# Performance work log

Hardware: AMD Instinct MI355X
Metric: run time of the kernel (lower is better)

## Reference

```python
import jax, jax.numpy as jnp
import numpy as np

B = 65536
HID = 256
C_K, C_V, C_S, NQ = 4, 8, 4, 4
EMB_OUT = 64  # state_embedding_size - 1


def _spatial_basis():
    # h = w = 5, U = V = 2 -> [5,5,4] Fourier basis
    ph = jnp.arange(1.0, 6.0)[:, None] * jnp.ones((1, 5)) * (np.pi / 5.0)
    pw = jnp.ones((5, 1)) * jnp.arange(1.0, 6.0)[None, :] * (np.pi / 5.0)
    u = jnp.arange(1.0, 3.0)[None, :]
    a = jnp.cos(ph[:, :, None] * u)  # [5,5,2]
    b = jnp.cos(pw[:, :, None] * u)  # [5,5,2]
    return jnp.einsum('hwu,hwv->hwuv', a, b).reshape(5, 5, 4).astype(jnp.float32)


def _conv(x, w, b):
    # x: NHWC, w: HWIO, pad=1, stride=1
    y = jax.lax.conv_general_dilated(x, w, window_strides=(1, 1), padding=[(1, 1), (1, 1)],
                                     dimension_numbers=('NHWC', 'HWIO', 'NHWC'))
    return y + b


def setup_inputs() -> dict:
    key = jax.random.key(0)
    ks = jax.random.split(key, 20)
    s = 0.05
    inp = {
        'X': jax.random.normal(ks[0], (B, 7, 7, 3), jnp.float32),
        'upper_module_hidden_state': jax.random.normal(ks[1], (B, HID), jnp.float32),
        'c1_w': jax.random.normal(ks[2], (5, 5, 3, 8), jnp.float32) * s,
        'c1_b': jax.random.normal(ks[3], (8,), jnp.float32) * s,
        'c2_w': jax.random.normal(ks[4], (3, 3, 8, 12), jnp.float32) * s,
        'c2_b': jax.random.normal(ks[5], (12,), jnp.float32) * s,
    }
    qdims = [(HID, 256), (256, 128), (128, 64), (64, 32), (32, 32)]
    for i, (din, dout) in enumerate(qdims):
        inp[f'qw{i}'] = jax.random.normal(ks[6 + 2 * i], (din, dout), jnp.float32) * s
        inp[f'qb{i}'] = jax.random.normal(ks[7 + 2 * i], (dout,), jnp.float32) * s
    inp['aw0'] = jax.random.normal(ks[16], ((C_V + C_S) * NQ, 32), jnp.float32) * s
    inp['ab0'] = jax.random.normal(ks[17], (32,), jnp.float32) * s
    inp['aw1'] = jax.random.normal(ks[18], (32, EMB_OUT), jnp.float32) * s
    inp['ab1'] = jax.random.normal(ks[19], (EMB_OUT,), jnp.float32) * s
    return inp


def reference(X, upper_module_hidden_state, c1_w, c1_b, c2_w, c2_b,
              qw0, qb0, qw1, qb1, qw2, qb2, qw3, qb3, qw4, qb4,
              aw0, ab0, aw1, ab1):
    b = X.shape[0]
    # vision CNN: [b,7,7,3] -> [b,5,5,8] -> [b,5,5,12]
    O = _conv(_conv(X, c1_w, c1_b), c2_w, c2_b)
    K, V = O[..., :C_K], O[..., C_K:]
    S = jnp.broadcast_to(_spatial_basis(), (b, 5, 5, C_S))
    K = jnp.concatenate([K, S], axis=-1)  # [b,5,5,8]
    V = jnp.concatenate([V, S], axis=-1)  # [b,5,5,12]
    # query MLP -> [b,4,8]
    q = upper_module_hidden_state
    for w, bi in [(qw0, qb0), (qw1, qb1), (qw2, qb2), (qw3, qb3)]:
        q = jax.nn.relu(q @ w + bi)
    q = (q @ qw4 + qb4).reshape(-1, NQ, C_K + C_S)
    # attention logits over 25 spatial positions, softmax over space
    A = jnp.einsum('bhwk,bqk->bhwq', K, q).reshape(b, 25, NQ)
    A = jax.nn.softmax(A, axis=1)
    # apply_alpha: [b,nq,25] @ [b,25,12] -> [b,nq,12]; chunk+cat == reshape
    a = jnp.einsum('bpq,bpd->bqd', A, V.reshape(b, 25, C_V + C_S)).reshape(b, NQ * (C_V + C_S))
    # answer MLP
    return jax.nn.relu(a @ aw0 + ab0) @ aw1 + ab1
```

## Files before the change

kernel.cpp:

```cpp
#include <hip/hip_runtime.h>
#include <hip/hip_bf16.h>

#define NB 65536

typedef __attribute__((ext_vector_type(8))) short short8;
typedef __attribute__((ext_vector_type(4))) short short4v;
typedef __attribute__((ext_vector_type(4))) float f32x4;
typedef __attribute__((ext_vector_type(16))) float f32x16;
typedef __attribute__((ext_vector_type(4))) unsigned int u32x4;

__device__ inline short f2bf(float f) {
    unsigned u = __builtin_bit_cast(unsigned, f);
    unsigned r = (u + 0x7fffu + ((u >> 16) & 1u)) >> 16;
    return (short)(unsigned short)r;
}
__device__ inline float b2f(short s) {
    return __builtin_bit_cast(float, (unsigned)((unsigned short)s) << 16);
}
__device__ inline unsigned pkbf(float lo, float hi) {
    return ((unsigned)(unsigned short)f2bf(hi) << 16) | (unsigned)(unsigned short)f2bf(lo);
}

#define MLPW_CNT 109568
#define WEFF_CNT 51200
#define A0 (MLPW_CNT + WEFF_CNT + 320)
#define A1 (A0 + 2048)
#define A2 (A1 + 2048)
#define A3 (A2 + 100)
#define PREP_TOT (A3 + 512)


__global__ void __launch_bounds__(256) prep_kernel(
    const float* __restrict__ w0, const float* __restrict__ w1,
    const float* __restrict__ w2, const float* __restrict__ w3,
    const float* __restrict__ w4,
    const float* __restrict__ b0, const float* __restrict__ b1,
    const float* __restrict__ b2, const float* __restrict__ b3,
    const float* __restrict__ b4,
    const float* __restrict__ c1w, const float* __restrict__ c1b,
    const float* __restrict__ c2w, const float* __restrict__ c2b,
    const float* __restrict__ aw0, const float* __restrict__ aw1,
    short* __restrict__ wt, short* __restrict__ weff, float* __restrict__ beff,
    short* __restrict__ aw0T, short* __restrict__ aw1T, float* __restrict__ sTab,
    float* __restrict__ biasP)
{
    int idx = blockIdx.x * 256 + threadIdx.x;
    if (idx < MLPW_CNT) {
        const float* W; int N, KT, base;
        if (idx < 65536)       { W = w0; N = 256; KT = 16; base = 0; }
        else if (idx < 98304)  { W = w1; N = 128; KT = 16; base = 65536; }
        else if (idx < 106496) { W = w2; N = 64;  KT = 8;  base = 98304; }
        else if (idx < 108544) { W = w3; N = 32;  KT = 4;  base = 106496; }
        else                   { W = w4; N = 32;  KT = 2;  base = 108544; }
        int i  = idx - base;
        int nt = i / (KT * 512);
        int r1 = i - nt * (KT * 512);
        int kt = r1 >> 9;
        int l  = (r1 & 511) >> 3;
        int j  = i & 7;
        int n  = nt * 32 + (l & 31);
        int k  = kt * 16 + ((l >> 5) << 3) + j;
        wt[idx] = f2bf(W[k * N + n]);
    } else if (idx < MLPW_CNT + WEFF_CNT) {
        int it = idx - MLPW_CNT;
        int n = it / 160, k = it - n * 160;
        float acc = 0.f;
        if (n < 300 && k < 147) {
            int oc = n % 12, p = n / 12, oy = p / 5, ox = p - oy * 5;
            int ci = k % 3,  t = k / 3, iy = t / 7, ix = t - iy * 7;
            for (int y = 0; y < 5; ++y) {
                int ky = iy - y + 1, ly = y - oy + 1;
                if ((unsigned)ky < 5u && (unsigned)ly < 3u) {
                    for (int x = 0; x < 5; ++x) {
                        int kx = ix - x + 1, lx = x - ox + 1;
                        if ((unsigned)kx < 5u && (unsigned)lx < 3u) {
                            const float* p1 = c1w + ((ky * 5 + kx) * 3 + ci) * 8;
                            const float* p2 = c2w + ((ly * 3 + lx) * 8) * 12 + oc;
#pragma unroll
                            for (int c = 0; c < 8; ++c) acc += p1[c] * p2[c * 12];
                        }
                    }
                }
            }
        }
        weff[it] = f2bf(acc);
    } else if (idx < A0) {
        int n = idx - MLPW_CNT - WEFF_CNT;
        float acc = 0.f;
        if (n < 300) {
            int oc = n % 12, p = n / 12, oy = p / 5, ox = p - oy * 5;
            acc = c2b[oc];
            for (int y = 0; y < 5; ++y) {
                int ly = y - oy + 1;
                if ((unsigned)ly < 3u) {
                    for (int x = 0; x < 5; ++x) {
                        int lx = x - ox + 1;
                        if ((unsigned)lx < 3u) {
#pragma unroll
                            for (int c = 0; c < 8; ++c)
                                acc += c2w[((ly * 3 + lx) * 8 + c) * 12 + oc] * c1b[c];
                        }
                    }
                }
            }
        }
        beff[n] = acc;
    } else if (idx < A1) {
        int t = idx - A0;
        int n = t >> 6, k = t & 63;
        aw0T[t] = (k < 48) ? f2bf(aw0[k * 32 + n]) : (short)0;
    } else if (idx < A2) {
        int t = idx - A1;
        int n = t >> 5, k = t & 31;
        aw1T[t] = f2bf(aw1[k * 64 + n]);
    } else if (idx < A3) {
        int i = idx - A2;
        int p = i >> 2, s = i & 3;
        int h = p / 5, w = p - 5 * h;
        int u = (s >> 1) + 1, v = (s & 1) + 1;
        const float PI5 = 0.6283185307179586f;
        sTab[i] = cosf(((float)(h + 1) * PI5) * (float)u) *
                  cosf(((float)(w + 1) * PI5) * (float)v);
    } else if (idx < PREP_TOT) {
        int t = idx - A3;
        const float* B; int N, base;
        if (t < 256)      { B = b0; N = 256; base = 0; }
        else if (t < 384) { B = b1; N = 128; base = 256; }
        else if (t < 448) { B = b2; N = 64;  base = 384; }
        else if (t < 480) { B = b3; N = 32;  base = 448; }
        else              { B = b4; N = 32;  base = 480; }
        int u  = t - base;
        int h  = u / (N / 2);
        int w  = u - h * (N / 2);
        int nt = w >> 4, r = w & 15;
        biasP[t] = B[nt * 32 + (r & 3) + 8 * (r >> 2) + 4 * h];
    }
}

template<int K, int N, bool RELU>
__device__ inline void layerR(const short* __restrict__ wp,
                              const float* __restrict__ bp,
                              const u32x4* __restrict__ inF,
                              u32x4* __restrict__ outF,
                              int lane, int h)
{
    constexpr int KT = K / 16, NT = N / 32;
#pragma unroll
    for (int nt = 0; nt < NT; ++nt) {
        f32x16 a;
#pragma unroll
        for (int r = 0; r < 16; ++r) a[r] = 0.f;
#pragma unroll
        for (int kt = 0; kt < KT; ++kt) {
            short8 wf = *(const short8*)(wp + (nt * KT + kt) * 512 + lane * 8);
            a = __builtin_amdgcn_mfma_f32_32x32x16_bf16(
                    wf, __builtin_bit_cast(short8, inF[kt]), a, 0, 0, 0);
        }
        const float* bpp = bp + h * (N / 2) + nt * 16;
        unsigned q[8];
#pragma unroll
        for (int i = 0; i < 8; ++i) {
            float v0 = a[2 * i] + bpp[2 * i];
            float v1 = a[2 * i + 1] + bpp[2 * i + 1];
            if (RELU) { v0 = fmaxf(v0, 0.f); v1 = fmaxf(v1, 0.f); }
            q[i] = pkbf(v0, v1);
        }
        unsigned xq[8];
#pragma unroll
        for (int i = 0; i < 8; ++i) xq[i] = (unsigned)__shfl_xor((int)q[i], 32, 64);
        u32x4 fa, fb;
        if (h == 0) {
            fa[0] = q[0];  fa[1] = q[1];  fa[2] = xq[0]; fa[3] = xq[1];
            fb[0] = q[4];  fb[1] = q[5];  fb[2] = xq[4]; fb[3] = xq[5];
        } else {
            fa[0] = xq[2]; fa[1] = xq[3]; fa[2] = q[2];  fa[3] = q[3];
            fb[0] = xq[6]; fb[1] = xq[7]; fb[2] = q[6];  fb[3] = q[7];
        }
        outF[2 * nt]     = fa;
        outF[2 * nt + 1] = fb;
    }
}

template<int K>
__device__ inline void layerQ(const short* __restrict__ wp,
                              const float* __restrict__ bp,
                              const u32x4* __restrict__ inF,
                              short* __restrict__ qout,
                              int lane, int h, int r0)
{
    constexpr int KT = K / 16;
    f32x16 a;
#pragma unroll
    for (int r = 0; r < 16; ++r) a[r] = 0.f;
#pragma unroll
    for (int kt = 0; kt < KT; ++kt) {
        short8 wf = *(const short8*)(wp + kt * 512 + lane * 8);
        a = __builtin_amdgcn_mfma_f32_32x32x16_bf16(
                wf, __builtin_bit_cast(short8, inF[kt]), a, 0, 0, 0);
    }
    const float* bpp = bp + h * 16;
    short* qb = qout + (size_t)(r0 + (lane & 31)) * 32 + 4 * h;
    const int fo[8] = {0, 2, 8, 10, 16, 18, 24, 26};
#pragma unroll
    for (int i = 0; i < 8; ++i) {
        float v0 = a[2 * i] + bpp[2 * i];
        float v1 = a[2 * i + 1] + bpp[2 * i + 1];
        *(unsigned*)(qb + fo[i]) = pkbf(v0, v1);
    }
}

__global__ void __launch_bounds__(64, 2) mlp_kernel(
    const float* __restrict__ hid,
    const short* __restrict__ wp,
    const float* __restrict__ biasP,
    short* __restrict__ qout)
{
    const int lane = threadIdx.x;
    const int h = lane >> 5, b = lane & 31;
    const int r0 = blockIdx.x * 32;

    u32x4 A[16], B[16], C[8], D[4], E[2];
    const float* hb = hid + (size_t)(r0 + b) * 256 + h * 8;
#pragma unroll
    for (int kt = 0; kt < 16; ++kt) {
        float4 x = *(const float4*)(hb + kt * 16);
        float4 y = *(const float4*)(hb + kt * 16 + 4);
        u32x4 f;
        f[0] = pkbf(x.x, x.y); f[1] = pkbf(x.z, x.w);
        f[2] = pkbf(y.x, y.y); f[3] = pkbf(y.z, y.w);
        A[kt] = f;
    }
    layerR<256, 256, true>(wp,          biasP,       A, B, lane, h);
    layerR<256, 128, true>(wp + 65536,  biasP + 256, B, C, lane, h);
    layerR<128,  64, true>(wp + 98304,  biasP + 384, C, D, lane, h);
    layerR< 64,  32, true>(wp + 106496, biasP + 448, D, E, lane, h);
    layerQ< 32>           (wp + 108544, biasP + 480, E, qout, lane, h, r0);
}

__global__ void __launch_bounds__(64) conv_attn_kernel(
    const float* __restrict__ Xg,
    const short* __restrict__ weffT,
    const float* __restrict__ beff,
    const short* __restrict__ aw0T, const float* __restrict__ ab0,
    const short* __restrict__ aw1T, const float* __restrict__ ab1,
    const float* __restrict__ sTab,
    const short* __restrict__ qb16,
    float* __restrict__ out)
{
    __shared__ __align__(16) unsigned char spool[14096];
    short* sKc = (short*)spool;
    short* sVc = (short*)(spool + 3200);
    short* sX  = (short*)spool;
    short* sQ  = (short*)(spool + 9600);
    float* sS  = (float*)(spool + 10624);
    short* sA  = (short*)(spool + 11024);
    short* sH  = (short*)(spool + 13072);

    const int lane   = threadIdx.x;
    const int lanelo = lane & 15;
    const int g      = lane >> 4;
    const int blk    = blockIdx.x;

    {
        short8 qv = *(const short8*)(qb16 + blk * 512 + lane * 8);
        *(short8*)(sQ + lane * 8) = qv;
    }
    if (lane < 50) {
        float2 t = *(const float2*)(sTab + lane * 2);
        sS[lane * 2]     = t.x;
        sS[lane * 2 + 1] = t.y;
    }
#pragma unroll
    for (int i = 0; i < 4; ++i) {
        int t = lane + i * 64;
        if (t < 208) {
            int r = t / 13, c = 147 + (t - r * 13);
            int ch = c >> 3;
            sX[r * 192 + ((ch ^ (r & 7)) << 3) + (c & 7)] = 0;
        }
    }
    {
        const float* xb = Xg + (size_t)blk * 2352;
#define PUTX(IDX, F) { int _i = (IDX); int _r = _i / 147; int _c = _i - _r * 147; \
        int _ch = _c >> 3; sX[_r * 192 + ((_ch ^ (_r & 7)) << 3) + (_c & 7)] = f2bf(F); }
#pragma unroll
        for (int i = 0; i < 10; ++i) {
            int idx4 = lane + i * 64;
            if (idx4 < 588) {
                float4 v = reinterpret_cast<const float4*>(xb)[idx4];
                int base = idx4 * 4;
                PUTX(base + 0, v.x)
                PUTX(base + 1, v.y)
                PUTX(base + 2, v.z)
                PUTX(base + 3, v.w)
            }
        }
#undef PUTX
    }

    short8 af[5];
#pragma unroll
    for (int kt = 0; kt < 5; ++kt) {
        int phys = (kt * 4 + g) ^ (lanelo & 7);
        af[kt] = *(const short8*)(sX + lanelo * 192 + phys * 8);
    }

    short8 bf[2][5];
    {
        const short* wb = weffT + lanelo * 160 + g * 8;
#pragma unroll
        for (int kt = 0; kt < 5; ++kt) bf[0][kt] = *(const short8*)(wb + kt * 32);
    }
#pragma unroll
    for (int nt = 0; nt < 19; ++nt) {
        if (nt + 1 < 19) {
            const short* wb = weffT + ((nt + 1) * 16 + lanelo) * 160 + g * 8;
#pragma unroll
            for (int kt = 0; kt < 5; ++kt)
                bf[(nt + 1) & 1][kt] = *(const short8*)(wb + kt * 32);
        }
        f32x4 a; a[0] = 0.f; a[1] = 0.f; a[2] = 0.f; a[3] = 0.f;
#pragma unroll
        for (int kt = 0; kt < 5; ++kt)
            a = __builtin_amdgcn_mfma_f32_16x16x32_bf16(af[kt], bf[nt & 1][kt], a, 0, 0, 0);
        int n = nt * 16 + lanelo;
        if (n < 300) {
            float bb = beff[n];
            int p = n / 12, c = n - p * 12;
#pragma unroll
            for (int j = 0; j < 4; ++j) {
                int el = g * 4 + j;
                float v = a[j] + bb;
                if (c < 4) sKc[el * 100 + p * 4 + c]       = f2bf(v);
                else       sVc[el * 200 + p * 8 + (c - 4)] = f2bf(v);
            }
        }
    }

    {
        const int el = lane >> 2, qi = lane & 3;
        short8 qv = *(const short8*)(sQ + el * 32 + qi * 8);
        float qf[8];
#pragma unroll
        for (int i = 0; i < 8; ++i) qf[i] = b2f(qv[i]);

        float lg[25];
        float mx = -1e30f;
#pragma unroll
        for (int p = 0; p < 25; ++p) {
            short4v kv = *(const short4v*)(sKc + el * 100 + p * 4);
            const float* sp = sS + p * 4;
            float s = b2f(kv[0]) * qf[0] + b2f(kv[1]) * qf[1]
                    + b2f(kv[2]) * qf[2] + b2f(kv[3]) * qf[3]
                    + sp[0] * qf[4] + sp[1] * qf[5]
                    + sp[2] * qf[6] + sp[3] * qf[7];
            lg[p] = s;
            mx = fmaxf(mx, s);
        }
        float sum = 0.f;
#pragma unroll
        for (int p = 0; p < 25; ++p) { lg[p] = __expf(lg[p] - mx); sum += lg[p]; }
        float inv = 1.f / sum;

        float o[12];
#pragma unroll
        for (int d = 0; d < 12; ++d) o[d] = 0.f;
#pragma unroll
        for (int p = 0; p < 25; ++p) {
            float w = lg[p];
            short4v v0 = *(const short4v*)(sVc + el * 200 + p * 8);
            short4v v1 = *(const short4v*)(sVc + el * 200 + p * 8 + 4);
            const float* sp = sS + p * 4;
            o[0] += w * b2f(v0[0]); o[1] += w * b2f(v0[1]);
            o[2] += w * b2f(v0[2]); o[3] += w * b2f(v0[3]);
            o[4] += w * b2f(v1[0]); o[5] += w * b2f(v1[1]);
            o[6] += w * b2f(v1[2]); o[7] += w * b2f(v1[3]);
            o[8]  += w * sp[0]; o[9]  += w * sp[1];
            o[10] += w * sp[2]; o[11] += w * sp[3];
        }
#pragma unroll
        for (int d = 0; d < 12; ++d) {
            int col = qi * 12 + d;
            int ch = col >> 3;
            sA[el * 64 + ((ch ^ (el & 7)) << 3) + (col & 7)] = f2bf(o[d] * inv);
        }
#pragma unroll
        for (int t = 0; t < 4; ++t) {
            int col = 48 + qi * 4 + t;
            int ch = col >> 3;
            sA[el * 64 + ((ch ^ (el & 7)) << 3) + (col & 7)] = 0;
        }
    }

    {
        short8 aa0, aa1;
        {
            int p0 = (0 * 4 + g) ^ (lanelo & 7);
            int p1 = (1 * 4 + g) ^ (lanelo & 7);
            aa0 = *(const short8*)(sA + lanelo * 64 + p0 * 8);
            aa1 = *(const short8*)(sA + lanelo * 64 + p1 * 8);
        }
#pragma unroll
        for (int nt2 = 0; nt2 < 2; ++nt2) {
            int n = nt2 * 16 + lanelo;
            short8 bw0 = *(const short8*)(aw0T + n * 64 + g * 8);
            short8 bw1 = *(const short8*)(aw0T + n * 64 + 32 + g * 8);
            f32x4 hh; hh[0] = 0.f; hh[1] = 0.f; hh[2] = 0.f; hh[3] = 0.f;
            hh = __builtin_amdgcn_mfma_f32_16x16x32_bf16(aa0, bw0, hh, 0, 0, 0);
            hh = __builtin_amdgcn_mfma_f32_16x16x32_bf16(aa1, bw1, hh, 0, 0, 0);
            float bb = ab0[n];
#pragma unroll
            for (int j = 0; j < 4; ++j) {
                int row = g * 4 + j;
                int ch = n >> 3;
                float v = fmaxf(hh[j] + bb, 0.f);
                sH[row * 32 + ((ch ^ (row & 3)) << 3) + (n & 7)] = f2bf(v);
            }
        }
    }

    {
        short8 ah;
        {
            int ph = (g ^ (lanelo & 3));
            ah = *(const short8*)(sH + lanelo * 32 + ph * 8);
        }
#pragma unroll
        for (int nt3 = 0; nt3 < 4; ++nt3) {
            int n = nt3 * 16 + lanelo;
            short8 bw = *(const short8*)(aw1T + n * 32 + g * 8);
            f32x4 oacc; oacc[0] = 0.f; oacc[1] = 0.f; oacc[2] = 0.f; oacc[3] = 0.f;
            oacc = __builtin_amdgcn_mfma_f32_16x16x32_bf16(ah, bw, oacc, 0, 0, 0);
            float bb = ab1[n];
#pragma unroll
            for (int j = 0; j < 4; ++j) {
                int el = g * 4 + j;
                out[((size_t)blk * 16 + el) * 64 + n] = oacc[j] + bb;
            }
        }
    }
}


extern "C" void kernel_launch(void* const* d_in, const int* in_sizes, int n_in,
                              void* d_out, int out_size, void* d_ws, size_t ws_size,
                              hipStream_t stream)
{
    const float* X   = (const float*)d_in[0];
    const float* hid = (const float*)d_in[1];
    const float* c1w = (const float*)d_in[2];
    const float* c1b = (const float*)d_in[3];
    const float* c2w = (const float*)d_in[4];
    const float* c2b = (const float*)d_in[5];
    const float* qw0 = (const float*)d_in[6];
    const float* qb0 = (const float*)d_in[7];
    const float* qw1 = (const float*)d_in[8];
    const float* qb1 = (const float*)d_in[9];
    const float* qw2 = (const float*)d_in[10];
    const float* qb2 = (const float*)d_in[11];
    const float* qw3 = (const float*)d_in[12];
    const float* qb3 = (const float*)d_in[13];
    const float* qw4 = (const float*)d_in[14];
    const float* qb4 = (const float*)d_in[15];
    const float* aw0 = (const float*)d_in[16];
    const float* ab0 = (const float*)d_in[17];
    const float* aw1 = (const float*)d_in[18];
    const float* ab1 = (const float*)d_in[19];

    float* out   = (float*)d_out;
    short* qb16  = (short*)d_ws;
    short* wsW   = qb16 + (size_t)NB * 32;
    short* weffT = wsW + MLPW_CNT;
    float* beff  = (float*)(weffT + WEFF_CNT);
    short* aw0T  = (short*)(beff + 320);
    short* aw1T  = aw0T + 2048;
    float* sTab  = (float*)(aw1T + 2048);
    float* biasP = sTab + 100;

    hipLaunchKernelGGL(prep_kernel, dim3((PREP_TOT + 255) / 256), dim3(256), 0, stream,
                       qw0, qw1, qw2, qw3, qw4, qb0, qb1, qb2, qb3, qb4,
                       c1w, c1b, c2w, c2b, aw0, aw1,
                       wsW, weffT, beff, aw0T, aw1T, sTab, biasP);
    hipLaunchKernelGGL(mlp_kernel, dim3(NB / 32), dim3(64), 0, stream,
                       hid, wsW, biasP, qb16);
    hipLaunchKernelGGL(conv_attn_kernel, dim3(NB / 16), dim3(64), 0, stream,
                       X, weffT, beff, aw0T, ab0, aw1T, ab1, sTab, qb16, out);
}
```

Baseline: 89.47 us.

## Process two 16-element tiles per conv_attn block to reuse conv weights

The conv/attention kernel now handles 32 batch elements per 64-thread block instead of 16. Each loaded conv weight fragment feeds two MFMAs, one per tile, and weight prefetch is deepened to triple buffering. The grid is halved, and the query and spatial-table staging through shared memory is replaced with direct global loads. In exchange, register pressure and shared memory per block roughly double, with a launch-bounds hint of two blocks, which may reduce occupancy.

```diff
diff --git a/kernel.cpp b/kernel.cpp
--- a/kernel.cpp
+++ b/kernel.cpp
@@ -237,7 +237,7 @@
     layerQ< 32>           (wp + 108544, biasP + 480, E, qout, lane, h, r0);
 }
 
-__global__ void __launch_bounds__(64) conv_attn_kernel(
+__global__ void __launch_bounds__(64, 2) conv_attn_kernel(
     const float* __restrict__ Xg,
     const short* __restrict__ weffT,
     const float* __restrict__ beff,
@@ -247,40 +247,28 @@
     const short* __restrict__ qb16,
     float* __restrict__ out)
 {
-    __shared__ __align__(16) unsigned char spool[14096];
-    short* sKc = (short*)spool;
-    short* sVc = (short*)(spool + 3200);
-    short* sX  = (short*)spool;
-    short* sQ  = (short*)(spool + 9600);
-    float* sS  = (float*)(spool + 10624);
-    short* sA  = (short*)(spool + 11024);
-    short* sH  = (short*)(spool + 13072);
+    __shared__ __align__(16) short sKV[2][4800];
+    __shared__ __align__(16) short sA[2][1024];
+    __shared__ __align__(16) short sH[2][512];
 
     const int lane   = threadIdx.x;
     const int lanelo = lane & 15;
     const int g      = lane >> 4;
     const int blk    = blockIdx.x;
 
-    {
-        short8 qv = *(const short8*)(qb16 + blk * 512 + lane * 8);
-        *(short8*)(sQ + lane * 8) = qv;
-    }
-    if (lane < 50) {
-        float2 t = *(const float2*)(sTab + lane * 2);
-        sS[lane * 2]     = t.x;
-        sS[lane * 2 + 1] = t.y;
-    }
-#pragma unroll
-    for (int i = 0; i < 4; ++i) {
-        int t = lane + i * 64;
-        if (t < 208) {
-            int r = t / 13, c = 147 + (t - r * 13);
-            int ch = c >> 3;
-            sX[r * 192 + ((ch ^ (r & 7)) << 3) + (c & 7)] = 0;
-        }
-    }
-    {
-        const float* xb = Xg + (size_t)blk * 2352;
+#pragma unroll
+    for (int t = 0; t < 2; ++t) {
+        short* sX = &sKV[t][0];
+#pragma unroll
+        for (int i = 0; i < 4; ++i) {
+            int tt = lane + i * 64;
+            if (tt < 208) {
+                int r = tt / 13, c = 147 + (tt - r * 13);
+                int ch = c >> 3;
+                sX[r * 192 + ((ch ^ (r & 7)) << 3) + (c & 7)] = 0;
+            }
+        }
+        const float* xb = Xg + (size_t)blk * 4704 + t * 2352;
 #define PUTX(IDX, F) { int _i = (IDX); int _r = _i / 147; int _c = _i - _r * 147; \
         int _ch = _c >> 3; sX[_r * 192 + ((_ch ^ (_r & 7)) << 3) + (_c & 7)] = f2bf(F); }
 #pragma unroll
@@ -298,48 +286,68 @@
 #undef PUTX
     }
 
-    short8 af[5];
+    short8 af0[5], af1[5];
 #pragma unroll
     for (int kt = 0; kt < 5; ++kt) {
         int phys = (kt * 4 + g) ^ (lanelo & 7);
-        af[kt] = *(const short8*)(sX + lanelo * 192 + phys * 8);
-    }
-
-    short8 bf[2][5];
+        af0[kt] = *(const short8*)(&sKV[0][0] + lanelo * 192 + phys * 8);
+        af1[kt] = *(const short8*)(&sKV[1][0] + lanelo * 192 + phys * 8);
+    }
+
+    short8 bf[3][5];
     {
-        const short* wb = weffT + lanelo * 160 + g * 8;
-#pragma unroll
-        for (int kt = 0; kt < 5; ++kt) bf[0][kt] = *(const short8*)(wb + kt * 32);
+        const short* wb0 = weffT + lanelo * 160 + g * 8;
+        const short* wb1 = weffT + (16 + lanelo) * 160 + g * 8;
+#pragma unroll
+        for (int kt = 0; kt < 5; ++kt) {
+            bf[0][kt] = *(const short8*)(wb0 + kt * 32);
+            bf[1][kt] = *(const short8*)(wb1 + kt * 32);
+        }
     }
 #pragma unroll
     for (int nt = 0; nt < 19; ++nt) {
-        if (nt + 1 < 19) {
-            const short* wb = weffT + ((nt + 1) * 16 + lanelo) * 160 + g * 8;
+        if (nt + 2 < 19) {
+            const short* wb = weffT + ((nt + 2) * 16 + lanelo) * 160 + g * 8;
 #pragma unroll
             for (int kt = 0; kt < 5; ++kt)
-                bf[(nt + 1) & 1][kt] = *(const short8*)(wb + kt * 32);
-        }
-        f32x4 a; a[0] = 0.f; a[1] = 0.f; a[2] = 0.f; a[3] = 0.f;
-#pragma unroll
-        for (int kt = 0; kt < 5; ++kt)
-            a = __builtin_amdgcn_mfma_f32_16x16x32_bf16(af[kt], bf[nt & 1][kt], a, 0, 0, 0);
+                bf[(nt + 2) % 3][kt] = *(const short8*)(wb + kt * 32);
+        }
+        f32x4 a0, a1;
+        a0[0] = 0.f; a0[1] = 0.f; a0[2] = 0.f; a0[3] = 0.f;
+        a1[0] = 0.f; a1[1] = 0.f; a1[2] = 0.f; a1[3] = 0.f;
+#pragma unroll
+        for (int kt = 0; kt < 5; ++kt) {
+            a0 = __builtin_amdgcn_mfma_f32_16x16x32_bf16(af0[kt], bf[nt % 3][kt], a0, 0, 0, 0);
+            a1 = __builtin_amdgcn_mfma_f32_16x16x32_bf16(af1[kt], bf[nt % 3][kt], a1, 0, 0, 0);
+        }
         int n = nt * 16 + lanelo;
         if (n < 300) {
             float bb = beff[n];
             int p = n / 12, c = n - p * 12;
+            int kidx = p * 4 + c;
+            int vidx = 1600 + p * 8 + (c - 4);
 #pragma unroll
             for (int j = 0; j < 4; ++j) {
                 int el = g * 4 + j;
-                float v = a[j] + bb;
-                if (c < 4) sKc[el * 100 + p * 4 + c]       = f2bf(v);
-                else       sVc[el * 200 + p * 8 + (c - 4)] = f2bf(v);
-            }
-        }
-    }
-
-    {
+                float v0 = a0[j] + bb;
+                float v1 = a1[j] + bb;
+                if (c < 4) {
+                    sKV[0][el * 100 + kidx] = f2bf(v0);
+                    sKV[1][el * 100 + kidx] = f2bf(v1);
+                } else {
+                    sKV[0][el * 200 + vidx] = f2bf(v0);
+                    sKV[1][el * 200 + vidx] = f2bf(v1);
+                }
+            }
+        }
+    }
+
+#pragma unroll
+    for (int t = 0; t < 2; ++t) {
+        const short* sKc = &sKV[t][0];
+        const short* sVc = &sKV[t][1600];
         const int el = lane >> 2, qi = lane & 3;
-        short8 qv = *(const short8*)(sQ + el * 32 + qi * 8);
+        short8 qv = *(const short8*)(qb16 + (size_t)(blk * 32 + t * 16 + el) * 32 + qi * 8);
         float qf[8];
 #pragma unroll
         for (int i = 0; i < 8; ++i) qf[i] = b2f(qv[i]);
@@ -349,11 +357,11 @@
 #pragma unroll
         for (int p = 0; p < 25; ++p) {
             short4v kv = *(const short4v*)(sKc + el * 100 + p * 4);
-            const float* sp = sS + p * 4;
+            float4 sv = *(const float4*)(sTab + p * 4);
             float s = b2f(kv[0]) * qf[0] + b2f(kv[1]) * qf[1]
                     + b2f(kv[2]) * qf[2] + b2f(kv[3]) * qf[3]
-                    + sp[0] * qf[4] + sp[1] * qf[5]
-                    + sp[2] * qf[6] + sp[3] * qf[7];
+                    + sv.x * qf[4] + sv.y * qf[5]
+                    + sv.z * qf[6] + sv.w * qf[7];
             lg[p] = s;
             mx = fmaxf(mx, s);
         }
@@ -370,35 +378,36 @@
             float w = lg[p];
             short4v v0 = *(const short4v*)(sVc + el * 200 + p * 8);
             short4v v1 = *(const short4v*)(sVc + el * 200 + p * 8 + 4);
-            const float* sp = sS + p * 4;
+            float4 sv = *(const float4*)(sTab + p * 4);
             o[0] += w * b2f(v0[0]); o[1] += w * b2f(v0[1]);
             o[2] += w * b2f(v0[2]); o[3] += w * b2f(v0[3]);
             o[4] += w * b2f(v1[0]); o[5] += w * b2f(v1[1]);
             o[6] += w * b2f(v1[2]); o[7] += w * b2f(v1[3]);
-            o[8]  += w * sp[0]; o[9]  += w * sp[1];
-            o[10] += w * sp[2]; o[11] += w * sp[3];
+            o[8]  += w * sv.x; o[9]  += w * sv.y;
+            o[10] += w * sv.z; o[11] += w * sv.w;
         }
 #pragma unroll
         for (int d = 0; d < 12; ++d) {
             int col = qi * 12 + d;
             int ch = col >> 3;
-            sA[el * 64 + ((ch ^ (el & 7)) << 3) + (col & 7)] = f2bf(o[d] * inv);
-        }
-#pragma unroll
-        for (int t = 0; t < 4; ++t) {
-            int col = 48 + qi * 4 + t;
+            sA[t][el * 64 + ((ch ^ (el & 7)) << 3) + (col & 7)] = f2bf(o[d] * inv);
+        }
+#pragma unroll
+        for (int z = 0; z < 4; ++z) {
+            int col = 48 + qi * 4 + z;
             int ch = col >> 3;
-            sA[el * 64 + ((ch ^ (el & 7)) << 3) + (col & 7)] = 0;
-        }
-    }
-
-    {
+            sA[t][el * 64 + ((ch ^ (el & 7)) << 3) + (col & 7)] = 0;
+        }
+    }
+
+#pragma unroll
+    for (int t = 0; t < 2; ++t) {
         short8 aa0, aa1;
         {
             int p0 = (0 * 4 + g) ^ (lanelo & 7);
             int p1 = (1 * 4 + g) ^ (lanelo & 7);
-            aa0 = *(const short8*)(sA + lanelo * 64 + p0 * 8);
-            aa1 = *(const short8*)(sA + lanelo * 64 + p1 * 8);
+            aa0 = *(const short8*)(&sA[t][0] + lanelo * 64 + p0 * 8);
+            aa1 = *(const short8*)(&sA[t][0] + lanelo * 64 + p1 * 8);
         }
 #pragma unroll
         for (int nt2 = 0; nt2 < 2; ++nt2) {
@@ -414,16 +423,17 @@
                 int row = g * 4 + j;
                 int ch = n >> 3;
                 float v = fmaxf(hh[j] + bb, 0.f);
-                sH[row * 32 + ((ch ^ (row & 3)) << 3) + (n & 7)] = f2bf(v);
-            }
-        }
-    }
-
-    {
+                sH[t][row * 32 + ((ch ^ (row & 3)) << 3) + (n & 7)] = f2bf(v);
+            }
+        }
+    }
+
+#pragma unroll
+    for (int t = 0; t < 2; ++t) {
         short8 ah;
         {
             int ph = (g ^ (lanelo & 3));
-            ah = *(const short8*)(sH + lanelo * 32 + ph * 8);
+            ah = *(const short8*)(&sH[t][0] + lanelo * 32 + ph * 8);
         }
 #pragma unroll
         for (int nt3 = 0; nt3 < 4; ++nt3) {
@@ -435,7 +445,7 @@
 #pragma unroll
             for (int j = 0; j < 4; ++j) {
                 int el = g * 4 + j;
-                out[((size_t)blk * 16 + el) * 64 + n] = oacc[j] + bb;
+                out[((size_t)blk * 32 + t * 16 + el) * 64 + n] = oacc[j] + bb;
             }
         }
     }
@@ -483,6 +493,6 @@
                        wsW, weffT, beff, aw0T, aw1T, sTab, biasP);
     hipLaunchKernelGGL(mlp_kernel, dim3(NB / 32), dim3(64), 0, stream,
                        hid, wsW, biasP, qb16);
-    hipLaunchKernelGGL(conv_attn_kernel, dim3(NB / 16), dim3(64), 0, stream,
+    hipLaunchKernelGGL(conv_attn_kernel, dim3(NB / 32), dim3(64), 0, stream,
                        X, weffT, beff, aw0T, ab0, aw1T, ab1, sTab, qb16, out);
 }
```

Measured after the change: 95.93 us. +7.2%, slower.

## Pack four independent waves per conv-attention block and deepen weight prefetch

Applied to the files above, without the earlier changes.

The conv/attention kernel now launches 256-thread blocks in which each of four waves handles its own 16 elements, using per-wave shared buffers. The q vectors and the spatial basis table are read directly from global memory instead of being staged in LDS. The weight B-fragment prefetch in the conv MFMA loop goes from double to triple buffering. The aim is fewer, larger blocks with better latency hiding, at the cost of more registers and more shared memory per block, which may limit occupancy.

```diff
diff --git a/kernel.cpp b/kernel.cpp
--- a/kernel.cpp
+++ b/kernel.cpp
@@ -237,7 +237,7 @@
     layerQ< 32>           (wp + 108544, biasP + 480, E, qout, lane, h, r0);
 }
 
-__global__ void __launch_bounds__(64) conv_attn_kernel(
+__global__ void __launch_bounds__(256, 4) conv_attn_kernel(
     const float* __restrict__ Xg,
     const short* __restrict__ weffT,
     const float* __restrict__ beff,
@@ -247,29 +247,21 @@
     const short* __restrict__ qb16,
     float* __restrict__ out)
 {
-    __shared__ __align__(16) unsigned char spool[14096];
-    short* sKc = (short*)spool;
-    short* sVc = (short*)(spool + 3200);
-    short* sX  = (short*)spool;
-    short* sQ  = (short*)(spool + 9600);
-    float* sS  = (float*)(spool + 10624);
-    short* sA  = (short*)(spool + 11024);
-    short* sH  = (short*)(spool + 13072);
-
-    const int lane   = threadIdx.x;
+    __shared__ __align__(16) short sKV[4][4800];
+    __shared__ __align__(16) short sA[4][1024];
+    __shared__ __align__(16) short sH[4][512];
+
+    const int tid    = threadIdx.x;
+    const int w      = tid >> 6;
+    const int lane   = tid & 63;
     const int lanelo = lane & 15;
     const int g      = lane >> 4;
-    const int blk    = blockIdx.x;
-
-    {
-        short8 qv = *(const short8*)(qb16 + blk * 512 + lane * 8);
-        *(short8*)(sQ + lane * 8) = qv;
-    }
-    if (lane < 50) {
-        float2 t = *(const float2*)(sTab + lane * 2);
-        sS[lane * 2]     = t.x;
-        sS[lane * 2 + 1] = t.y;
-    }
+    const int e0     = blockIdx.x * 64 + w * 16;
+
+    short* sX  = &sKV[w][0];
+    short* sKc = &sKV[w][0];
+    short* sVc = &sKV[w][1600];
+
 #pragma unroll
     for (int i = 0; i < 4; ++i) {
         int t = lane + i * 64;
@@ -280,7 +272,7 @@
         }
     }
     {
-        const float* xb = Xg + (size_t)blk * 2352;
+        const float* xb = Xg + (size_t)e0 * 147;
 #define PUTX(IDX, F) { int _i = (IDX); int _r = _i / 147; int _c = _i - _r * 147; \
         int _ch = _c >> 3; sX[_r * 192 + ((_ch ^ (_r & 7)) << 3) + (_c & 7)] = f2bf(F); }
 #pragma unroll
@@ -305,24 +297,28 @@
         af[kt] = *(const short8*)(sX + lanelo * 192 + phys * 8);
     }
 
-    short8 bf[2][5];
+    short8 bf[3][5];
     {
-        const short* wb = weffT + lanelo * 160 + g * 8;
-#pragma unroll
-        for (int kt = 0; kt < 5; ++kt) bf[0][kt] = *(const short8*)(wb + kt * 32);
+        const short* wb0 = weffT + lanelo * 160 + g * 8;
+        const short* wb1 = weffT + (16 + lanelo) * 160 + g * 8;
+#pragma unroll
+        for (int kt = 0; kt < 5; ++kt) {
+            bf[0][kt] = *(const short8*)(wb0 + kt * 32);
+            bf[1][kt] = *(const short8*)(wb1 + kt * 32);
+        }
     }
 #pragma unroll
     for (int nt = 0; nt < 19; ++nt) {
-        if (nt + 1 < 19) {
-            const short* wb = weffT + ((nt + 1) * 16 + lanelo) * 160 + g * 8;
+        if (nt + 2 < 19) {
+            const short* wb = weffT + ((nt + 2) * 16 + lanelo) * 160 + g * 8;
 #pragma unroll
             for (int kt = 0; kt < 5; ++kt)
-                bf[(nt + 1) & 1][kt] = *(const short8*)(wb + kt * 32);
+                bf[(nt + 2) % 3][kt] = *(const short8*)(wb + kt * 32);
         }
         f32x4 a; a[0] = 0.f; a[1] = 0.f; a[2] = 0.f; a[3] = 0.f;
 #pragma unroll
         for (int kt = 0; kt < 5; ++kt)
-            a = __builtin_amdgcn_mfma_f32_16x16x32_bf16(af[kt], bf[nt & 1][kt], a, 0, 0, 0);
+            a = __builtin_amdgcn_mfma_f32_16x16x32_bf16(af[kt], bf[nt % 3][kt], a, 0, 0, 0);
         int n = nt * 16 + lanelo;
         if (n < 300) {
             float bb = beff[n];
@@ -339,7 +335,7 @@
 
     {
         const int el = lane >> 2, qi = lane & 3;
-        short8 qv = *(const short8*)(sQ + el * 32 + qi * 8);
+        short8 qv = *(const short8*)(qb16 + (size_t)(e0 + el) * 32 + qi * 8);
         float qf[8];
 #pragma unroll
         for (int i = 0; i < 8; ++i) qf[i] = b2f(qv[i]);
@@ -349,11 +345,11 @@
 #pragma unroll
         for (int p = 0; p < 25; ++p) {
             short4v kv = *(const short4v*)(sKc + el * 100 + p * 4);
-            const float* sp = sS + p * 4;
+            float4 sv = *(const float4*)(sTab + p * 4);
             float s = b2f(kv[0]) * qf[0] + b2f(kv[1]) * qf[1]
                     + b2f(kv[2]) * qf[2] + b2f(kv[3]) * qf[3]
-                    + sp[0] * qf[4] + sp[1] * qf[5]
-                    + sp[2] * qf[6] + sp[3] * qf[7];
+                    + sv.x * qf[4] + sv.y * qf[5]
+                    + sv.z * qf[6] + sv.w * qf[7];
             lg[p] = s;
             mx = fmaxf(mx, s);
         }
@@ -367,28 +363,28 @@
         for (int d = 0; d < 12; ++d) o[d] = 0.f;
 #pragma unroll
         for (int p = 0; p < 25; ++p) {
-            float w = lg[p];
+            float wgt = lg[p];
             short4v v0 = *(const short4v*)(sVc + el * 200 + p * 8);
             short4v v1 = *(const short4v*)(sVc + el * 200 + p * 8 + 4);
-            const float* sp = sS + p * 4;
-            o[0] += w * b2f(v0[0]); o[1] += w * b2f(v0[1]);
-            o[2] += w * b2f(v0[2]); o[3] += w * b2f(v0[3]);
-            o[4] += w * b2f(v1[0]); o[5] += w * b2f(v1[1]);
-            o[6] += w * b2f(v1[2]); o[7] += w * b2f(v1[3]);
-            o[8]  += w * sp[0]; o[9]  += w * sp[1];
-            o[10] += w * sp[2]; o[11] += w * sp[3];
+            float4 sv = *(const float4*)(sTab + p * 4);
+            o[0] += wgt * b2f(v0[0]); o[1] += wgt * b2f(v0[1]);
+            o[2] += wgt * b2f(v0[2]); o[3] += wgt * b2f(v0[3]);
+            o[4] += wgt * b2f(v1[0]); o[5] += wgt * b2f(v1[1]);
+            o[6] += wgt * b2f(v1[2]); o[7] += wgt * b2f(v1[3]);
+            o[8]  += wgt * sv.x; o[9]  += wgt * sv.y;
+            o[10] += wgt * sv.z; o[11] += wgt * sv.w;
         }
 #pragma unroll
         for (int d = 0; d < 12; ++d) {
             int col = qi * 12 + d;
             int ch = col >> 3;
-            sA[el * 64 + ((ch ^ (el & 7)) << 3) + (col & 7)] = f2bf(o[d] * inv);
-        }
-#pragma unroll
-        for (int t = 0; t < 4; ++t) {
-            int col = 48 + qi * 4 + t;
+            sA[w][el * 64 + ((ch ^ (el & 7)) << 3) + (col & 7)] = f2bf(o[d] * inv);
+        }
+#pragma unroll
+        for (int z = 0; z < 4; ++z) {
+            int col = 48 + qi * 4 + z;
             int ch = col >> 3;
-            sA[el * 64 + ((ch ^ (el & 7)) << 3) + (col & 7)] = 0;
+            sA[w][el * 64 + ((ch ^ (el & 7)) << 3) + (col & 7)] = 0;
         }
     }
 
@@ -397,8 +393,8 @@
         {
             int p0 = (0 * 4 + g) ^ (lanelo & 7);
             int p1 = (1 * 4 + g) ^ (lanelo & 7);
-            aa0 = *(const short8*)(sA + lanelo * 64 + p0 * 8);
-            aa1 = *(const short8*)(sA + lanelo * 64 + p1 * 8);
+            aa0 = *(const short8*)(&sA[w][0] + lanelo * 64 + p0 * 8);
+            aa1 = *(const short8*)(&sA[w][0] + lanelo * 64 + p1 * 8);
         }
 #pragma unroll
         for (int nt2 = 0; nt2 < 2; ++nt2) {
@@ -414,7 +410,7 @@
                 int row = g * 4 + j;
                 int ch = n >> 3;
                 float v = fmaxf(hh[j] + bb, 0.f);
-                sH[row * 32 + ((ch ^ (row & 3)) << 3) + (n & 7)] = f2bf(v);
+                sH[w][row * 32 + ((ch ^ (row & 3)) << 3) + (n & 7)] = f2bf(v);
             }
         }
     }
@@ -423,7 +419,7 @@
         short8 ah;
         {
             int ph = (g ^ (lanelo & 3));
-            ah = *(const short8*)(sH + lanelo * 32 + ph * 8);
+            ah = *(const short8*)(&sH[w][0] + lanelo * 32 + ph * 8);
         }
 #pragma unroll
         for (int nt3 = 0; nt3 < 4; ++nt3) {
@@ -435,7 +431,7 @@
 #pragma unroll
             for (int j = 0; j < 4; ++j) {
                 int el = g * 4 + j;
-                out[((size_t)blk * 16 + el) * 64 + n] = oacc[j] + bb;
+                out[((size_t)e0 + el) * 64 + n] = oacc[j] + bb;
             }
         }
     }
@@ -483,6 +479,6 @@
                        wsW, weffT, beff, aw0T, aw1T, sTab, biasP);
     hipLaunchKernelGGL(mlp_kernel, dim3(NB / 32), dim3(64), 0, stream,
                        hid, wsW, biasP, qb16);
-    hipLaunchKernelGGL(conv_attn_kernel, dim3(NB / 16), dim3(64), 0, stream,
+    hipLaunchKernelGGL(conv_attn_kernel, dim3(NB / 64), dim3(256), 0, stream,
                        X, weffT, beff, aw0T, ab0, aw1T, ab1, sTab, qb16, out);
 }
```

Result: faster. 82.98 us (-7.3%).
